# Performance work log

Hardware: AMD Instinct MI355X
Metric: run time of the kernel (lower is better)

The kernel has to match this reference:

```python
import jax, jax.numpy as jnp
import numpy as np

B, S, H, FD, P = 32, 512, 768, 64, 30  # batch, seq, hidden(768 fixed), fusion_dim, proj(30 fixed)


def setup_inputs() -> dict:
    key = jax.random.key(0)
    ks = jax.random.split(key, 6)
    return {
        "hidden_states": jax.random.normal(ks[0], (B, S, H), jnp.float32),
        "audio_data": jax.random.normal(ks[1], (B, S, FD), jnp.float32),
        "attention_mask": jnp.zeros((B, 1, 1, S), jnp.float32),  # BERT extended mask, 0 = attend
        "W_t": jax.random.normal(ks[2], (P, H), jnp.float32) * 0.02,   # Conv1d(768,30,k=1) weight
        "W_a": jax.random.normal(ks[3], (P, FD), jnp.float32) * 0.02,  # Conv1d(fusion_dim,30,k=1) weight
        "text_w": jnp.ones((1,), jnp.float32),
        "audio_w": jnp.ones((1,), jnp.float32),
        "fusion_b": jnp.zeros((1,), jnp.float32),
        "W_dense": jax.random.normal(ks[4], (H, H), jnp.float32) * 0.02,  # Linear(768,768), [out,in]
        "b_dense": jnp.zeros((H,), jnp.float32),
        "ln_w": jnp.ones((H,), jnp.float32),
        "ln_b": jnp.zeros((H,), jnp.float32),
    }


def reference(hidden_states, audio_data, attention_mask, W_t, W_a,
              text_w, audio_w, fusion_b, W_dense, b_dense, ln_w, ln_b):
    # attention_mask.squeeze(1) -> [B,1,S]; permute(0,2,1) -> [B,S,1]
    mask = attention_mask[:, 0]                     # [B,1,S]
    mask_t = jnp.transpose(mask, (0, 2, 1))         # [B,S,1]

    # proj_t: Conv1d k=1 == per-position linear
    text = jnp.einsum('bsh,ph->bsp', hidden_states, W_t)      # [B,S,30]
    # original detaches this normalizer (numpy path)
    norm = jax.lax.stop_gradient(jnp.sqrt(jnp.linalg.norm(text.reshape(-1))))
    text = text / norm

    audio = jnp.einsum('bsf,pf->bsp', audio_data, W_a)        # [B,S,30]

    text_att1 = jax.nn.relu(jnp.einsum('bsp,btp->bst', text, text))    # [B,S,S]
    audio_att = jax.nn.relu(jnp.einsum('bsp,btp->bst', audio, audio))  # [B,S,S]

    fusion_att_raw = text_w * text_att1 + audio_w * audio_att + fusion_b
    fusion_att1 = jax.nn.relu(fusion_att_raw)

    att = jax.nn.softmax(fusion_att_raw + mask + mask_t, axis=-1)      # [B,S,S]
    fusion_data = jnp.einsum('bst,bth->bsh', att, hidden_states) + hidden_states

    h = fusion_data @ W_dense.T + b_dense                              # [B,S,768]
    # BertLayerNorm (TF-style, eps inside sqrt)
    u = h.mean(-1, keepdims=True)
    s = ((h - u) ** 2).mean(-1, keepdims=True)
    h = ln_w * (h - u) / jnp.sqrt(s + 1e-12) + ln_b

    return (h[:, 0], text_att1, fusion_att1)
```

## Files before the change

### kernel.cpp

```cpp
#include <hip/hip_runtime.h>
#include <math.h>

#define BB 32
#define SS 512
#define HH 768
#define FDD 64
#define PP 30
#define NR 16384

typedef __attribute__((ext_vector_type(8))) short short8v;
typedef __attribute__((ext_vector_type(4))) float f32x4;

#define O_TEXTF  0u
#define O_AUDF   524288u
#define O_ATT    1048576u
#define O_FPART  1081344u
#define O_WDT    1572864u
#define O_WTB    2162688u
#define O_WAB    2174976u
#define O_TEXTB  2176000u
#define O_AUDB   2438144u
#define O_SUMSQ  2700288u

__device__ __forceinline__ unsigned short f2bf(float f){
  unsigned u = __float_as_uint(f);
  unsigned r = (u + 0x7fffu + ((u>>16)&1u)) >> 16;
  return (unsigned short)r;
}
__device__ __forceinline__ short8v pack8(const float4& p0, const float4& p1){
  union { short8v v; unsigned u[4]; } r;
  r.u[0] = f2bf(p0.x) | ((unsigned)f2bf(p0.y) << 16);
  r.u[1] = f2bf(p0.z) | ((unsigned)f2bf(p0.w) << 16);
  r.u[2] = f2bf(p1.x) | ((unsigned)f2bf(p1.y) << 16);
  r.u[3] = f2bf(p1.z) | ((unsigned)f2bf(p1.w) << 16);
  return r.v;
}

__global__ __launch_bounds__(256) void k_prep(const float* __restrict__ Wd,
    const float* __restrict__ Wt, const float* __restrict__ Wa, float* __restrict__ ws){
  const int bi = blockIdx.x, tid = threadIdx.x;
  if (bi < 576){
    __shared__ float L[32][33];
    const int tx = bi % 24, ty = bi / 24;
    const int lx = tid & 31, ly = tid >> 5;
    #pragma unroll
    for (int i = 0; i < 4; ++i)
      L[ly + i*8][lx] = Wd[(size_t)(ty*32 + ly + i*8)*HH + tx*32 + lx];
    __syncthreads();
    #pragma unroll
    for (int i = 0; i < 4; ++i)
      ws[O_WDT + (size_t)(tx*32 + ly + i*8)*HH + ty*32 + lx] = L[lx][ly + i*8];
  } else if (bi < 680){
    int idx = (bi - 576)*256 + tid;
    if (idx < 24576){
      int j = idx & 7, lane = (idx>>3) & 63, t = idx>>9;
      int n = t / 24, ks = t - n*24;
      int p = n*16 + (lane & 15);
      int k = ks*32 + ((lane>>4)<<3) + j;
      float v = (p < PP) ? Wt[p*HH + k] : 0.0f;
      ((unsigned short*)(ws + O_WTB))[idx] = f2bf(v);
    } else {
      int fa = idx - 24576;
      int j = fa & 7, lane = (fa>>3) & 63, t = fa>>9;
      int n = t>>1, ks = t & 1;
      int p = n*16 + (lane & 15);
      int k = ks*32 + ((lane>>4)<<3) + j;
      float v = (p < PP) ? Wa[p*FDD + k] : 0.0f;
      ((unsigned short*)(ws + O_WAB))[fa] = f2bf(v);
    }
  } else if (tid == 0){
    ws[O_SUMSQ] = 0.0f;
  }
}

__global__ __launch_bounds__(256) void k_proj(const float* __restrict__ hs,
    const float* __restrict__ ad, float* __restrict__ ws){
  const int tid = threadIdx.x;
  const int lane = tid & 63, w = tid >> 6;
  const int rowbase = blockIdx.x * 64;
  const int mrow = rowbase + w*16 + (lane & 15);
  const int koff = (lane >> 4) << 3;
  const short8v* WTB = (const short8v*)(ws + O_WTB);
  const short8v* WAB = (const short8v*)(ws + O_WAB);
  f32x4 accT0 = {0,0,0,0}, accT1 = {0,0,0,0};

  const float* hp = hs + (size_t)mrow*HH + koff;
  #pragma unroll 4
  for (int ks = 0; ks < 24; ++ks){
    float4 p0 = *(const float4*)(hp + ks*32);
    float4 p1 = *(const float4*)(hp + ks*32 + 4);
    short8v a = pack8(p0, p1);
    accT0 = __builtin_amdgcn_mfma_f32_16x16x32_bf16(a, WTB[ks*64 + lane], accT0, 0, 0, 0);
    accT1 = __builtin_amdgcn_mfma_f32_16x16x32_bf16(a, WTB[(24 + ks)*64 + lane], accT1, 0, 0, 0);
  }

  f32x4 accA0 = {0,0,0,0}, accA1 = {0,0,0,0};
  const float* ap = ad + (size_t)mrow*FDD + koff;
  #pragma unroll
  for (int ks = 0; ks < 2; ++ks){
    float4 q0 = *(const float4*)(ap + ks*32);
    float4 q1 = *(const float4*)(ap + ks*32 + 4);
    short8v a = pack8(q0, q1);
    accA0 = __builtin_amdgcn_mfma_f32_16x16x32_bf16(a, WAB[ks*64 + lane], accA0, 0, 0, 0);
    accA1 = __builtin_amdgcn_mfma_f32_16x16x32_bf16(a, WAB[(2 + ks)*64 + lane], accA1, 0, 0, 0);
  }

  float* TF = ws + O_TEXTF;
  float* AF = ws + O_AUDF;
  unsigned short* TEXTB = (unsigned short*)(ws + O_TEXTB);
  unsigned short* AUDB  = (unsigned short*)(ws + O_AUDB);
  const int q4 = lane >> 4, pl = lane & 15;
  const int row0 = rowbase + w*16 + q4*4;
  float sq = 0.0f;
  #pragma unroll
  for (int r = 0; r < 4; ++r) sq += accT0[r]*accT0[r] + accT1[r]*accT1[r];
  *(float4*)(TF + (size_t)pl*NR + row0)      = *(float4*)&accT0;
  *(float4*)(TF + (size_t)(pl+16)*NR + row0) = *(float4*)&accT1;
  *(float4*)(AF + (size_t)pl*NR + row0)      = *(float4*)&accA0;
  *(float4*)(AF + (size_t)(pl+16)*NR + row0) = *(float4*)&accA1;
  #pragma unroll
  for (int r = 0; r < 4; ++r){
    int row = row0 + r;
    TEXTB[(size_t)row*32 + pl]      = f2bf(accT0[r]);
    TEXTB[(size_t)row*32 + 16 + pl] = f2bf(accT1[r]);
    AUDB[(size_t)row*32 + pl]       = f2bf(accA0[r]);
    AUDB[(size_t)row*32 + 16 + pl]  = f2bf(accA1[r]);
  }
  #pragma unroll
  for (int off = 32; off; off >>= 1) sq += __shfl_xor(sq, off);
  if (lane == 0) atomicAdd(ws + O_SUMSQ, sq);
}

__global__ __launch_bounds__(256) void k_gram(const float* __restrict__ ws,
    const float* __restrict__ twp, const float* __restrict__ awp, const float* __restrict__ fbp,
    float* __restrict__ out_text, float* __restrict__ out_fus){
  const int tid = threadIdx.x, lane = tid & 63, w = tid >> 6;
  const int tt = blockIdx.x, st = blockIdx.y, b = blockIdx.z;
  const unsigned short* TEXTB = (const unsigned short*)(ws + O_TEXTB);
  const unsigned short* AUDB  = (const unsigned short*)(ws + O_AUDB);
  const int q4 = lane >> 4, pl = lane & 15;
  const size_t srow  = (size_t)b*SS + st*64 + w*16 + pl;
  const size_t trow0 = (size_t)b*SS + tt*64 + pl;
  short8v at = *(const short8v*)&TEXTB[srow*32 + q4*8];
  short8v aa = *(const short8v*)&AUDB [srow*32 + q4*8];
  f32x4 z = {0,0,0,0};
  f32x4 ct[4], ca[4];
  #pragma unroll
  for (int n = 0; n < 4; ++n){
    short8v bt = *(const short8v*)&TEXTB[(trow0 + n*16)*32 + q4*8];
    short8v ba = *(const short8v*)&AUDB [(trow0 + n*16)*32 + q4*8];
    ct[n] = __builtin_amdgcn_mfma_f32_16x16x32_bf16(bt, at, z, 0, 0, 0);
    ca[n] = __builtin_amdgcn_mfma_f32_16x16x32_bf16(ba, aa, z, 0, 0, 0);
  }
  const float inv_s = 1.0f / sqrtf(ws[O_SUMSQ]);
  const float tw = twp[0], aw = awp[0], fb = fbp[0];
  const int s = st*64 + w*16 + pl;
  const int tbase = tt*64;
  #pragma unroll
  for (int n = 0; n < 4; ++n){
    float4 vt, vf;
    float* pt_ = (float*)&vt; float* pf_ = (float*)&vf;
    #pragma unroll
    for (int r = 0; r < 4; ++r){
      float t_ = fmaxf(ct[n][r]*inv_s, 0.0f);
      float a_ = fmaxf(ca[n][r], 0.0f);
      pt_[r] = t_;
      pf_[r] = fmaxf(tw*t_ + aw*a_ + fb, 0.0f);
    }
    size_t o = ((size_t)b*SS + s)*SS + tbase + n*16 + q4*4;
    *(float4*)(out_text + o) = vt;
    *(float4*)(out_fus  + o) = vf;
  }
}

__global__ __launch_bounds__(512) void k_att(float* __restrict__ ws, const float* __restrict__ amask,
    const float* __restrict__ twp, const float* __restrict__ awp, const float* __restrict__ fbp){
  const int b = blockIdx.x, tid = threadIdx.x;
  __shared__ float t0[32], a0[32];
  __shared__ float red[512];
  const float* TF = ws + O_TEXTF;
  const float* AF = ws + O_AUDF;
  if (tid < 32) t0[tid] = TF[(size_t)tid*NR + (size_t)b*SS];
  else if (tid < 64) a0[tid-32] = AF[(size_t)(tid-32)*NR + (size_t)b*SS];
  __syncthreads();
  const float inv_s = 1.0f / sqrtf(ws[O_SUMSQ]);
  const float tw = twp[0], aw = awp[0], fb = fbp[0];
  const float m0 = amask[(size_t)b*SS];
  const size_t base = (size_t)b*SS + tid;
  float dt = 0.f, da = 0.f;
  #pragma unroll
  for (int p = 0; p < 32; ++p){
    dt += t0[p]*TF[(size_t)p*NR + base];
    da += a0[p]*AF[(size_t)p*NR + base];
  }
  const float sv = tw*fmaxf(dt*inv_s, 0.f) + aw*fmaxf(da, 0.f) + fb
                 + amask[base] + m0;
  red[tid] = sv;
  __syncthreads();
  for (int s2 = 256; s2 > 0; s2 >>= 1){ if (tid < s2) red[tid] = fmaxf(red[tid], red[tid+s2]); __syncthreads(); }
  const float m = red[0];
  __syncthreads();
  const float e = __expf(sv - m);
  red[tid] = e;
  __syncthreads();
  for (int s2 = 256; s2 > 0; s2 >>= 1){ if (tid < s2) red[tid] += red[tid+s2]; __syncthreads(); }
  ws[O_ATT + base] = e / red[0];
}

__global__ __launch_bounds__(256) void k_pv(const float* __restrict__ hs, float* __restrict__ ws){
  const int tid = threadIdx.x;
  const int cx = blockIdx.x, th = blockIdx.y, b = blockIdx.z;
  __shared__ float a[64];
  if (tid < 64) a[tid] = ws[O_ATT + (size_t)b*SS + th*64 + tid];
  __syncthreads();
  const int c = cx*256 + tid;
  const float* hp = hs + ((size_t)b*SS + th*64)*HH + c;
  float acc = 0.f;
  #pragma unroll 8
  for (int t = 0; t < 64; ++t) acc += a[t]*hp[(size_t)t*HH];
  if (th == 0) acc += hs[(size_t)b*SS*HH + c];
  ws[O_FPART + ((size_t)th*BB + b)*HH + c] = acc;
}

__global__ __launch_bounds__(1024) void k_dense_ln(const float* __restrict__ ws,
    const float* __restrict__ bd, const float* __restrict__ lw, const float* __restrict__ lb,
    float* __restrict__ out){
  const int b = blockIdx.x, tid = threadIdx.x;
  __shared__ float f[HH];
  __shared__ float part[4*HH];
  __shared__ float red[1024];
  if (tid < HH){
    float s = 0.f;
    #pragma unroll
    for (int th = 0; th < 8; ++th) s += ws[O_FPART + ((size_t)th*BB + b)*HH + tid];
    f[tid] = s;
  }
  __syncthreads();
  const int cc = tid >> 8, o = tid & 255;
  const float* Wp = ws + O_WDT + (size_t)(cc*192)*HH;
  const float* fp = f + cc*192;
  float a0 = 0.f, a1 = 0.f, a2 = 0.f;
  #pragma unroll 8
  for (int i = 0; i < 192; ++i){
    const float fv = fp[i];
    const float* wr = Wp + (size_t)i*HH + o;
    a0 += fv*wr[0];
    a1 += fv*wr[256];
    a2 += fv*wr[512];
  }
  part[cc*HH + o]       = a0;
  part[cc*HH + o + 256] = a1;
  part[cc*HH + o + 512] = a2;
  __syncthreads();
  float h = 0.f;
  if (tid < HH)
    h = part[tid] + part[HH + tid] + part[2*HH + tid] + part[3*HH + tid] + bd[tid];
  red[tid] = (tid < HH) ? h : 0.f;
  __syncthreads();
  for (int s2 = 512; s2 > 0; s2 >>= 1){ if (tid < s2) red[tid] += red[tid+s2]; __syncthreads(); }
  const float u = red[0]*(1.0f/HH);
  __syncthreads();
  const float d = h - u;
  red[tid] = (tid < HH) ? d*d : 0.f;
  __syncthreads();
  for (int s2 = 512; s2 > 0; s2 >>= 1){ if (tid < s2) red[tid] += red[tid+s2]; __syncthreads(); }
  const float isd = 1.0f / sqrtf(red[0]*(1.0f/HH) + 1e-12f);
  if (tid < HH)
    out[(size_t)b*HH + tid] = lw[tid]*d*isd + lb[tid];
}

extern "C" void kernel_launch(void* const* d_in, const int* in_sizes, int n_in,
                              void* d_out, int out_size, void* d_ws, size_t ws_size,
                              hipStream_t stream){
  const float* hs    = (const float*)d_in[0];
  const float* ad    = (const float*)d_in[1];
  const float* amask = (const float*)d_in[2];
  const float* Wt    = (const float*)d_in[3];
  const float* Wa    = (const float*)d_in[4];
  const float* twp   = (const float*)d_in[5];
  const float* awp   = (const float*)d_in[6];
  const float* fbp   = (const float*)d_in[7];
  const float* Wd    = (const float*)d_in[8];
  const float* bd    = (const float*)d_in[9];
  const float* lw    = (const float*)d_in[10];
  const float* lb    = (const float*)d_in[11];
  float* out = (float*)d_out;
  float* ws  = (float*)d_ws;
  float* out_h    = out;
  float* out_text = out + (size_t)BB*HH;
  float* out_fus  = out_text + (size_t)BB*SS*SS;

  hipLaunchKernelGGL(k_prep, dim3(681), dim3(256), 0, stream, Wd, Wt, Wa, ws);
  hipLaunchKernelGGL(k_proj, dim3(NR/64), dim3(256), 0, stream, hs, ad, ws);
  hipLaunchKernelGGL(k_gram, dim3(8,8,BB), dim3(256), 0, stream, ws, twp, awp, fbp, out_text, out_fus);
  hipLaunchKernelGGL(k_att, dim3(BB), dim3(512), 0, stream, ws, amask, twp, awp, fbp);
  hipLaunchKernelGGL(k_pv, dim3(3,8,BB), dim3(256), 0, stream, hs, ws);
  hipLaunchKernelGGL(k_dense_ln, dim3(BB), dim3(1024), 0, stream, ws, bd, lw, lb, out_h);
}
```

Before: 186.8 us.

## Split dense+LayerNorm into K-chunked dense kernel and LN kernel; add nontemporal memory ops

The single 32-block dense+LayerNorm kernel becomes a 12x32-grid dense kernel that writes partial products per K chunk to workspace, followed by a small LayerNorm kernel that sums the partials. This spreads the W_dense reads over many more CUs. Streaming loads of hidden_states and the large gram output stores now use nontemporal hints to reduce cache pollution. The cost is an extra kernel launch and a workspace round trip for the partial sums.

```diff
diff --git a/kernel.cpp b/kernel.cpp
--- a/kernel.cpp
+++ b/kernel.cpp
@@ -15,6 +15,7 @@
 #define O_AUDF   524288u
 #define O_ATT    1048576u
 #define O_FPART  1081344u
+#define O_HPART  1277952u
 #define O_WDT    1572864u
 #define O_WTB    2162688u
 #define O_WAB    2174976u
@@ -27,12 +28,12 @@
   unsigned r = (u + 0x7fffu + ((u>>16)&1u)) >> 16;
   return (unsigned short)r;
 }
-__device__ __forceinline__ short8v pack8(const float4& p0, const float4& p1){
+__device__ __forceinline__ short8v pack8(const f32x4& p0, const f32x4& p1){
   union { short8v v; unsigned u[4]; } r;
-  r.u[0] = f2bf(p0.x) | ((unsigned)f2bf(p0.y) << 16);
-  r.u[1] = f2bf(p0.z) | ((unsigned)f2bf(p0.w) << 16);
-  r.u[2] = f2bf(p1.x) | ((unsigned)f2bf(p1.y) << 16);
-  r.u[3] = f2bf(p1.z) | ((unsigned)f2bf(p1.w) << 16);
+  r.u[0] = f2bf(p0[0]) | ((unsigned)f2bf(p0[1]) << 16);
+  r.u[1] = f2bf(p0[2]) | ((unsigned)f2bf(p0[3]) << 16);
+  r.u[2] = f2bf(p1[0]) | ((unsigned)f2bf(p1[1]) << 16);
+  r.u[3] = f2bf(p1[2]) | ((unsigned)f2bf(p1[3]) << 16);
   return r.v;
 }
 
@@ -84,22 +85,22 @@
   const short8v* WAB = (const short8v*)(ws + O_WAB);
   f32x4 accT0 = {0,0,0,0}, accT1 = {0,0,0,0};
 
-  const float* hp = hs + (size_t)mrow*HH + koff;
+  const f32x4* hp = (const f32x4*)(hs + (size_t)mrow*HH + koff);
   #pragma unroll 4
   for (int ks = 0; ks < 24; ++ks){
-    float4 p0 = *(const float4*)(hp + ks*32);
-    float4 p1 = *(const float4*)(hp + ks*32 + 4);
+    f32x4 p0 = __builtin_nontemporal_load(hp + ks*8);
+    f32x4 p1 = __builtin_nontemporal_load(hp + ks*8 + 1);
     short8v a = pack8(p0, p1);
     accT0 = __builtin_amdgcn_mfma_f32_16x16x32_bf16(a, WTB[ks*64 + lane], accT0, 0, 0, 0);
     accT1 = __builtin_amdgcn_mfma_f32_16x16x32_bf16(a, WTB[(24 + ks)*64 + lane], accT1, 0, 0, 0);
   }
 
   f32x4 accA0 = {0,0,0,0}, accA1 = {0,0,0,0};
-  const float* ap = ad + (size_t)mrow*FDD + koff;
+  const f32x4* ap = (const f32x4*)(ad + (size_t)mrow*FDD + koff);
   #pragma unroll
   for (int ks = 0; ks < 2; ++ks){
-    float4 q0 = *(const float4*)(ap + ks*32);
-    float4 q1 = *(const float4*)(ap + ks*32 + 4);
+    f32x4 q0 = __builtin_nontemporal_load(ap + ks*8);
+    f32x4 q1 = __builtin_nontemporal_load(ap + ks*8 + 1);
     short8v a = pack8(q0, q1);
     accA0 = __builtin_amdgcn_mfma_f32_16x16x32_bf16(a, WAB[ks*64 + lane], accA0, 0, 0, 0);
     accA1 = __builtin_amdgcn_mfma_f32_16x16x32_bf16(a, WAB[(2 + ks)*64 + lane], accA1, 0, 0, 0);
@@ -114,10 +115,10 @@
   float sq = 0.0f;
   #pragma unroll
   for (int r = 0; r < 4; ++r) sq += accT0[r]*accT0[r] + accT1[r]*accT1[r];
-  *(float4*)(TF + (size_t)pl*NR + row0)      = *(float4*)&accT0;
-  *(float4*)(TF + (size_t)(pl+16)*NR + row0) = *(float4*)&accT1;
-  *(float4*)(AF + (size_t)pl*NR + row0)      = *(float4*)&accA0;
-  *(float4*)(AF + (size_t)(pl+16)*NR + row0) = *(float4*)&accA1;
+  *(f32x4*)(TF + (size_t)pl*NR + row0)      = accT0;
+  *(f32x4*)(TF + (size_t)(pl+16)*NR + row0) = accT1;
+  *(f32x4*)(AF + (size_t)pl*NR + row0)      = accA0;
+  *(f32x4*)(AF + (size_t)(pl+16)*NR + row0) = accA1;
   #pragma unroll
   for (int r = 0; r < 4; ++r){
     int row = row0 + r;
@@ -158,18 +159,17 @@
   const int tbase = tt*64;
   #pragma unroll
   for (int n = 0; n < 4; ++n){
-    float4 vt, vf;
-    float* pt_ = (float*)&vt; float* pf_ = (float*)&vf;
+    f32x4 vt, vf;
     #pragma unroll
     for (int r = 0; r < 4; ++r){
       float t_ = fmaxf(ct[n][r]*inv_s, 0.0f);
       float a_ = fmaxf(ca[n][r], 0.0f);
-      pt_[r] = t_;
-      pf_[r] = fmaxf(tw*t_ + aw*a_ + fb, 0.0f);
+      vt[r] = t_;
+      vf[r] = fmaxf(tw*t_ + aw*a_ + fb, 0.0f);
     }
     size_t o = ((size_t)b*SS + s)*SS + tbase + n*16 + q4*4;
-    *(float4*)(out_text + o) = vt;
-    *(float4*)(out_fus  + o) = vf;
+    __builtin_nontemporal_store(vt, (f32x4*)(out_text + o));
+    __builtin_nontemporal_store(vf, (f32x4*)(out_fus  + o));
   }
 }
 
@@ -217,56 +217,64 @@
   const float* hp = hs + ((size_t)b*SS + th*64)*HH + c;
   float acc = 0.f;
   #pragma unroll 8
-  for (int t = 0; t < 64; ++t) acc += a[t]*hp[(size_t)t*HH];
+  for (int t = 0; t < 64; ++t) acc += a[t]*__builtin_nontemporal_load(hp + (size_t)t*HH);
   if (th == 0) acc += hs[(size_t)b*SS*HH + c];
   ws[O_FPART + ((size_t)th*BB + b)*HH + c] = acc;
 }
 
-__global__ __launch_bounds__(1024) void k_dense_ln(const float* __restrict__ ws,
+__global__ __launch_bounds__(256) void k_dense(float* __restrict__ ws){
+  const int kc = blockIdx.x, b = blockIdx.y, tid = threadIdx.x;
+  __shared__ float fc[64];
+  if (tid < 64){
+    float s = 0.f;
+    const int c = kc*64 + tid;
+    #pragma unroll
+    for (int th = 0; th < 8; ++th) s += ws[O_FPART + ((size_t)th*BB + b)*HH + c];
+    fc[tid] = s;
+  }
+  __syncthreads();
+  const float* Wp = ws + O_WDT + (size_t)(kc*64)*HH;
+  float a0 = 0.f, a1 = 0.f, a2 = 0.f;
+  #pragma unroll 8
+  for (int i = 0; i < 64; ++i){
+    const float fv = fc[i];
+    const float* wr = Wp + (size_t)i*HH + tid;
+    a0 += fv*wr[0];
+    a1 += fv*wr[256];
+    a2 += fv*wr[512];
+  }
+  float* hp = ws + O_HPART + ((size_t)kc*BB + b)*HH;
+  hp[tid]       = a0;
+  hp[tid + 256] = a1;
+  hp[tid + 512] = a2;
+}
+
+__global__ __launch_bounds__(256) void k_ln(const float* __restrict__ ws,
     const float* __restrict__ bd, const float* __restrict__ lw, const float* __restrict__ lb,
     float* __restrict__ out){
   const int b = blockIdx.x, tid = threadIdx.x;
-  __shared__ float f[HH];
-  __shared__ float part[4*HH];
-  __shared__ float red[1024];
-  if (tid < HH){
-    float s = 0.f;
-    #pragma unroll
-    for (int th = 0; th < 8; ++th) s += ws[O_FPART + ((size_t)th*BB + b)*HH + tid];
-    f[tid] = s;
-  }
-  __syncthreads();
-  const int cc = tid >> 8, o = tid & 255;
-  const float* Wp = ws + O_WDT + (size_t)(cc*192)*HH;
-  const float* fp = f + cc*192;
-  float a0 = 0.f, a1 = 0.f, a2 = 0.f;
-  #pragma unroll 8
-  for (int i = 0; i < 192; ++i){
-    const float fv = fp[i];
-    const float* wr = Wp + (size_t)i*HH + o;
-    a0 += fv*wr[0];
-    a1 += fv*wr[256];
-    a2 += fv*wr[512];
-  }
-  part[cc*HH + o]       = a0;
-  part[cc*HH + o + 256] = a1;
-  part[cc*HH + o + 512] = a2;
-  __syncthreads();
-  float h = 0.f;
-  if (tid < HH)
-    h = part[tid] + part[HH + tid] + part[2*HH + tid] + part[3*HH + tid] + bd[tid];
-  red[tid] = (tid < HH) ? h : 0.f;
-  __syncthreads();
-  for (int s2 = 512; s2 > 0; s2 >>= 1){ if (tid < s2) red[tid] += red[tid+s2]; __syncthreads(); }
+  __shared__ float red[256];
+  float a0 = bd[tid], a1 = bd[tid+256], a2 = bd[tid+512];
+  #pragma unroll
+  for (int kc = 0; kc < 12; ++kc){
+    const float* hp = ws + O_HPART + ((size_t)kc*BB + b)*HH;
+    a0 += hp[tid];
+    a1 += hp[tid + 256];
+    a2 += hp[tid + 512];
+  }
+  red[tid] = a0 + a1 + a2;
+  __syncthreads();
+  for (int s2 = 128; s2 > 0; s2 >>= 1){ if (tid < s2) red[tid] += red[tid+s2]; __syncthreads(); }
   const float u = red[0]*(1.0f/HH);
   __syncthreads();
-  const float d = h - u;
-  red[tid] = (tid < HH) ? d*d : 0.f;
-  __syncthreads();
-  for (int s2 = 512; s2 > 0; s2 >>= 1){ if (tid < s2) red[tid] += red[tid+s2]; __syncthreads(); }
+  const float d0 = a0-u, d1 = a1-u, d2 = a2-u;
+  red[tid] = d0*d0 + d1*d1 + d2*d2;
+  __syncthreads();
+  for (int s2 = 128; s2 > 0; s2 >>= 1){ if (tid < s2) red[tid] += red[tid+s2]; __syncthreads(); }
   const float isd = 1.0f / sqrtf(red[0]*(1.0f/HH) + 1e-12f);
-  if (tid < HH)
-    out[(size_t)b*HH + tid] = lw[tid]*d*isd + lb[tid];
+  out[(size_t)b*HH + tid]     = lw[tid]    *d0*isd + lb[tid];
+  out[(size_t)b*HH + tid+256] = lw[tid+256]*d1*isd + lb[tid+256];
+  out[(size_t)b*HH + tid+512] = lw[tid+512]*d2*isd + lb[tid+512];
 }
 
 extern "C" void kernel_launch(void* const* d_in, const int* in_sizes, int n_in,
@@ -295,5 +303,6 @@
   hipLaunchKernelGGL(k_gram, dim3(8,8,BB), dim3(256), 0, stream, ws, twp, awp, fbp, out_text, out_fus);
   hipLaunchKernelGGL(k_att, dim3(BB), dim3(512), 0, stream, ws, amask, twp, awp, fbp);
   hipLaunchKernelGGL(k_pv, dim3(3,8,BB), dim3(256), 0, stream, hs, ws);
-  hipLaunchKernelGGL(k_dense_ln, dim3(BB), dim3(1024), 0, stream, ws, bd, lw, lb, out_h);
-}
+  hipLaunchKernelGGL(k_dense, dim3(12,BB), dim3(256), 0, stream, ws);
+  hipLaunchKernelGGL(k_ln, dim3(BB), dim3(256), 0, stream, ws, bd, lw, lb, out_h);
+}
```

After: 182.3 us. 2.4% less time.
